# Performance work log

Measured on AMD Instinct MI355X. Metric: run time of the kernel, lower is better.

## Reference

```python
import jax, jax.numpy as jnp
import numpy as np

V, D, L, H, HKV, E = 32000, 1024, 4, 16, 4, 4
HD = D // H
B, T = 2, 1024
EPS = 1e-6
ROPE_BASE = 10000.0


def setup_inputs() -> dict:
    key = jax.random.key(0)
    ks = jax.random.split(key, 9)
    s = 0.02
    return {
        "input_ids": jax.random.randint(ks[0], (B, T), 0, V),
        "token_emb": jax.random.normal(ks[1], (V, D), jnp.float32) * s,
        "ln1_w": jnp.ones((L, D), jnp.float32),
        "q_w": jax.random.normal(ks[2], (L, D, D), jnp.float32) * s,
        "k_w": jax.random.normal(ks[3], (L, HKV * HD, D), jnp.float32) * s,
        "v_w": jax.random.normal(ks[4], (L, HKV * HD, D), jnp.float32) * s,
        "o_w": jax.random.normal(ks[5], (L, D, D), jnp.float32) * s,
        "ln2_w": jnp.ones((L, D), jnp.float32),
        "w1_w": jax.random.normal(ks[6], (L, E * D, D), jnp.float32) * s,
        "w2_w": jax.random.normal(ks[7], (L, D, E * D), jnp.float32) * s,
        "w3_w": jax.random.normal(ks[8], (L, E * D, D), jnp.float32) * s,
        "lnf_w": jnp.ones((D,), jnp.float32),
    }


def rmsnorm(x, w):
    var = jnp.mean(x * x, axis=-1, keepdims=True)
    return w * (x * jax.lax.rsqrt(var + EPS))


def rope_tables(t, dtype):
    inv_freq = 1.0 / (ROPE_BASE ** (jnp.arange(0, HD, 2, dtype=jnp.float32) / HD))
    freqs = jnp.outer(jnp.arange(t, dtype=jnp.float32), inv_freq)  # [T, HD/2]
    emb = jnp.concatenate([freqs, freqs], axis=-1)  # [T, HD]
    return emb.astype(dtype)[None, None], None  # placeholder shape helper


def rotate_half(x):
    x1, x2 = x[..., : HD // 2], x[..., HD // 2 :]
    return jnp.concatenate([-x2, x1], axis=-1)


def block(x, cos, sin, ln1, wq, wk, wv, wo, ln2, w1, w2, w3):
    # attention (pre-norm)
    h = rmsnorm(x, ln1)
    q = jnp.einsum('btd,ed->bte', h, wq).reshape(B, T, H, HD).transpose(0, 2, 1, 3)
    k = jnp.einsum('btd,ed->bte', h, wk).reshape(B, T, HKV, HD).transpose(0, 2, 1, 3)
    v = jnp.einsum('btd,ed->bte', h, wv).reshape(B, T, HKV, HD).transpose(0, 2, 1, 3)
    q = q * cos + rotate_half(q) * sin
    k = k * cos + rotate_half(k) * sin
    # GQA: repeat kv heads (repeat_interleave semantics)
    g = H // HKV
    k = jnp.repeat(k, g, axis=1)
    v = jnp.repeat(v, g, axis=1)
    scale = 1.0 / np.sqrt(HD)
    scores = jnp.einsum('bhqd,bhkd->bhqk', q, k) * scale
    causal = jnp.triu(jnp.ones((T, T), jnp.bool_), k=1)[None, None]
    scores = jnp.where(causal, -jnp.inf, scores)
    attn = jax.nn.softmax(scores.astype(jnp.float32), axis=-1).astype(q.dtype)
    o = jnp.einsum('bhqk,bhkd->bhqd', attn, v)
    o = o.transpose(0, 2, 1, 3).reshape(B, T, D)
    x = x + jnp.einsum('btd,ed->bte', o, wo)
    # SwiGLU FFN
    h = rmsnorm(x, ln2)
    gate = jax.nn.silu(jnp.einsum('btd,fd->btf', h, w1))
    up = jnp.einsum('btd,fd->btf', h, w3)
    x = x + jnp.einsum('btf,df->btd', gate * up, w2)
    return x


def forward(input_ids, token_emb, ln1_w, q_w, k_w, v_w, o_w, ln2_w, w1_w, w2_w, w3_w, lnf_w):
    x = token_emb[input_ids]  # [B,T,D]
    inv_freq = 1.0 / (ROPE_BASE ** (jnp.arange(0, HD, 2, dtype=jnp.float32) / HD))
    freqs = jnp.outer(jnp.arange(T, dtype=jnp.float32), inv_freq)
    emb = jnp.concatenate([freqs, freqs], axis=-1)  # [T, HD]
    cos = jnp.cos(emb)[None, None]  # [1,1,T,HD]
    sin = jnp.sin(emb)[None, None]
    for i in range(L):
        x = block(x, cos, sin, ln1_w[i], q_w[i], k_w[i], v_w[i], o_w[i],
                  ln2_w[i], w1_w[i], w2_w[i], w3_w[i])
    x = rmsnorm(x, lnf_w)
    logits = jnp.einsum('btd,vd->btv', x, token_emb)  # tied lm_head
    return logits


def reference(input_ids, token_emb, ln1_w, q_w, k_w, v_w, o_w, ln2_w, w1_w, w2_w, w3_w, lnf_w):
    return forward(input_ids, token_emb, ln1_w, q_w, k_w, v_w, o_w, ln2_w, w1_w, w2_w, w3_w, lnf_w)
```

## Files before the change

kernel.cpp:

```cpp
#include <hip/hip_runtime.h>
#include <math.h>

#define TT 1024
#define BB 2
#define DD 1024
#define NH 16
#define NKV 4
#define HD 64
#define ED 4096
#define LL 4
#define VV 32000
#define QKVS 1536

typedef __bf16 bf16x8 __attribute__((ext_vector_type(8)));
typedef float f32x4 __attribute__((ext_vector_type(4)));

__device__ inline unsigned short f2bf(float f) {
  unsigned u = __float_as_uint(f);
  u += 0x7fffu + ((u >> 16) & 1u);
  return (unsigned short)(u >> 16);
}

#define GLL16(gsrc, ldst)                                                            \
  __builtin_amdgcn_global_load_lds((const __attribute__((address_space(1))) void*)(gsrc), \
                                   (__attribute__((address_space(3))) void*)(ldst), 16, 0, 0)

__global__ void convw_kernel(const float* __restrict__ src, unsigned short* __restrict__ dst) {
  size_t i = (size_t)blockIdx.x * blockDim.x + threadIdx.x;
  float4 v = ((const float4*)src)[i];
  uint2 o;
  o.x = f2bf(v.x) | ((unsigned)f2bf(v.y) << 16);
  o.y = f2bf(v.z) | ((unsigned)f2bf(v.w) << 16);
  ((uint2*)dst)[i] = o;
}

__global__ void conv_qkv_kernel(const float* __restrict__ qw, const float* __restrict__ kw,
                                const float* __restrict__ vw, unsigned short* __restrict__ dst) {
  size_t i = (size_t)blockIdx.x * blockDim.x + threadIdx.x;
  size_t e = i * 4;
  int l = (int)(e / (QKVS * 1024));
  int rem = (int)(e - (size_t)l * (QKVS * 1024));
  int row = rem >> 10;
  int col = rem & 1023;
  const float* src;
  if (row < 1024) src = qw + (((size_t)l << 20) + ((size_t)row << 10)) + col;
  else if (row < 1280) src = kw + (((size_t)l << 18) + ((size_t)(row - 1024) << 10)) + col;
  else src = vw + (((size_t)l << 18) + ((size_t)(row - 1280) << 10)) + col;
  float4 v = *(const float4*)src;
  uint2 o;
  o.x = f2bf(v.x) | ((unsigned)f2bf(v.y) << 16);
  o.y = f2bf(v.z) | ((unsigned)f2bf(v.w) << 16);
  ((uint2*)dst)[i] = o;
}

__global__ void conv_w13_kernel(const float* __restrict__ w1, const float* __restrict__ w3,
                                unsigned short* __restrict__ dst) {
  size_t i = (size_t)blockIdx.x * blockDim.x + threadIdx.x;
  size_t e = i * 4;
  int l = (int)(e >> 23);
  int rem = (int)(e & ((1u << 23) - 1));
  int r = rem >> 10;
  int col = rem & 1023;
  int grp = r >> 4;
  int f = (grp >> 1) * 16 + (r & 15);
  const float* base = (grp & 1) ? w3 : w1;
  const float* src = base + (((size_t)l << 22) + ((size_t)f << 10)) + col;
  float4 v = *(const float4*)src;
  uint2 o;
  o.x = f2bf(v.x) | ((unsigned)f2bf(v.y) << 16);
  o.y = f2bf(v.z) | ((unsigned)f2bf(v.w) << 16);
  ((uint2*)dst)[i] = o;
}

__global__ void embed_kernel(const int* __restrict__ ids, const float* __restrict__ emb,
                             float* __restrict__ x) {
  int row = blockIdx.x;
  int id = ids[row];
  const float4* src = (const float4*)(emb + (size_t)id * DD);
  float4* dst = (float4*)(x + (size_t)row * DD);
  dst[threadIdx.x] = src[threadIdx.x];
}

__global__ __launch_bounds__(256) void rmsnorm_kernel(const float* __restrict__ x,
                                                      const float* __restrict__ wgt,
                                                      unsigned short* __restrict__ out) {
  int row = blockIdx.x;
  int tid = threadIdx.x;
  float4 v = *(const float4*)(x + (size_t)row * DD + tid * 4);
  float ss = v.x * v.x + v.y * v.y + v.z * v.z + v.w * v.w;
#pragma unroll
  for (int off = 32; off >= 1; off >>= 1) ss += __shfl_xor(ss, off);
  __shared__ float part[4];
  if ((tid & 63) == 0) part[tid >> 6] = ss;
  __syncthreads();
  ss = part[0] + part[1] + part[2] + part[3];
  float sc = rsqrtf(ss * (1.0f / DD) + 1e-6f);
  float4 wv = *(const float4*)(wgt + tid * 4);
  uint2 o;
  o.x = f2bf(v.x * wv.x * sc) | ((unsigned)f2bf(v.y * wv.y * sc) << 16);
  o.y = f2bf(v.z * wv.z * sc) | ((unsigned)f2bf(v.w * wv.w * sc) << 16);
  *(uint2*)(out + (size_t)row * DD + tid * 4) = o;
}

__global__ void add2_kernel(float* __restrict__ x, const float* __restrict__ p0,
                            const float* __restrict__ p1) {
  size_t i = (size_t)blockIdx.x * blockDim.x + threadIdx.x;
  float4 a = ((const float4*)x)[i];
  float4 b = ((const float4*)p0)[i];
  float4 c = ((const float4*)p1)[i];
  a.x += b.x + c.x; a.y += b.y + c.y; a.z += b.z + c.z; a.w += b.w + c.w;
  ((float4*)x)[i] = a;
}

template <int EPI>
__global__ __launch_bounds__(256) void gemm_bb(const unsigned short* __restrict__ A,
                                               const unsigned short* __restrict__ W,
                                               float* __restrict__ C,
                                               unsigned short* __restrict__ O2,
                                               int M, int N, int K) {
  __shared__ unsigned short As[128 * 32];
  __shared__ unsigned short Bs[128 * 32];
  const int tid = threadIdx.x;
  const int lane = tid & 63;
  const int w = tid >> 6;
  const int wm = (w >> 1) * 64;
  const int wn = (w & 1) * 64;
  const int l15 = lane & 15;
  const int quad = lane >> 4;
  const int q8 = quad * 8;

  const int nby = gridDim.y;
  const int nwg = gridDim.x * nby;
  const int bid = blockIdx.y * gridDim.x + blockIdx.x;
  int wk = bid;
  if ((nwg & 7) == 0) {
    int cpx = nwg >> 3;
    wk = (bid & 7) * cpx + (bid >> 3);
  }
  const int mBase = (wk % nby) * 128;
  const int nBase = (wk / nby) * 128;

  const int ksl = K / gridDim.z;
  const int kb0 = blockIdx.z * ksl;
  if (EPI == 0) C += (size_t)blockIdx.z * M * N;

  const unsigned short* Ab = A + (size_t)mBase * K;
  const unsigned short* Wb = W + (size_t)nBase * K;
  const int r0 = tid >> 2;
  const int c8 = (tid & 3) * 8;

  f32x4 acc[4][4] = {};

  for (int kt = kb0; kt < kb0 + ksl; kt += 32) {
    __syncthreads();
    GLL16(Ab + (size_t)r0 * K + kt + c8, As + (w * 64) * 8);
    GLL16(Ab + (size_t)(r0 + 64) * K + kt + c8, As + (256 + w * 64) * 8);
    GLL16(Wb + (size_t)r0 * K + kt + c8, Bs + (w * 64) * 8);
    GLL16(Wb + (size_t)(r0 + 64) * K + kt + c8, Bs + (256 + w * 64) * 8);
    __syncthreads();
    bf16x8 af[4], bfv[4];
#pragma unroll
    for (int ms = 0; ms < 4; ms++)
      af[ms] = *(const bf16x8*)&As[(wm + ms * 16 + l15) * 32 + q8];
#pragma unroll
    for (int ns = 0; ns < 4; ns++)
      bfv[ns] = *(const bf16x8*)&Bs[(wn + ns * 16 + l15) * 32 + q8];
#pragma unroll
    for (int ms = 0; ms < 4; ms++)
#pragma unroll
      for (int ns = 0; ns < 4; ns++)
        acc[ms][ns] = __builtin_amdgcn_mfma_f32_16x16x32_bf16(af[ms], bfv[ns], acc[ms][ns], 0, 0, 0);
  }

  if (EPI == 2) {
    const int fBase = ((nBase + wn) >> 5) * 16;
#pragma unroll
    for (int ms = 0; ms < 4; ms++)
#pragma unroll
      for (int r = 0; r < 4; r++) {
        int row = mBase + wm + ms * 16 + quad * 4 + r;
#pragma unroll
        for (int pp = 0; pp < 2; pp++) {
          float g = acc[ms][pp * 2][r];
          float u = acc[ms][pp * 2 + 1][r];
          float res = g / (1.f + __expf(-g)) * u;
          O2[(size_t)row * ED + fBase + pp * 16 + l15] = f2bf(res);
        }
      }
  } else if (EPI == 3) {
    const bool dorope = (nBase < 1280);
#pragma unroll
    for (int ms = 0; ms < 4; ms++)
#pragma unroll
      for (int r = 0; r < 4; r++) {
        int row = mBase + wm + ms * 16 + quad * 4 + r;
        float pos = (float)(row & (TT - 1));
#pragma unroll
        for (int ns = 0; ns < 2; ns++) {
          int col = nBase + wn + ns * 16 + l15;
          size_t i1 = (size_t)row * N + col;
          float x1 = acc[ms][ns][r], x2 = acc[ms][ns + 2][r];
          if (dorope) {
            int j = ns * 16 + l15;
            float invf = __expf(-(float)j * 0.28782313662f);
            float sv, cv;
            sincosf(pos * invf, &sv, &cv);
            C[i1] = x1 * cv - x2 * sv;
            C[i1 + 32] = x2 * cv + x1 * sv;
          } else {
            C[i1] = x1;
            C[i1 + 32] = x2;
          }
        }
      }
  } else {
#pragma unroll
    for (int ms = 0; ms < 4; ms++)
#pragma unroll
      for (int ns = 0; ns < 4; ns++)
#pragma unroll
        for (int r = 0; r < 4; r++) {
          int row = mBase + wm + ms * 16 + quad * 4 + r;
          int col = nBase + wn + ns * 16 + l15;
          size_t idx = (size_t)row * N + col;
          if (EPI == 0) C[idx] = acc[ms][ns][r];
          else if (EPI == 5) __builtin_nontemporal_store(acc[ms][ns][r], &C[idx]);
          else C[idx] += acc[ms][ns][r];
        }
  }
}

template <int EPI>
__global__ __launch_bounds__(256) void gemm_bt(const unsigned short* __restrict__ A,
                                               const float* __restrict__ W,
                                               float* __restrict__ C, int M, int N, int K) {
  __shared__ unsigned short As[128 * 40];
  __shared__ unsigned short Bs[128 * 40];
  const int tid = threadIdx.x;
  const int lane = tid & 63;
  const int w = tid >> 6;
  const int wm = (w >> 1) * 64;
  const int wn = (w & 1) * 64;
  const int l15 = lane & 15;
  const int quad = lane >> 4;
  const int q8 = quad * 8;

  const int nby = gridDim.y;
  const int nwg = gridDim.x * nby;
  const int bid = blockIdx.y * gridDim.x + blockIdx.x;
  int wk = bid;
  if ((nwg & 7) == 0) {
    int cpx = nwg >> 3;
    wk = (bid & 7) * cpx + (bid >> 3);
  }
  const int mBase = (wk % nby) * 128;
  const int nBase = (wk / nby) * 128;

  f32x4 acc[4][4] = {};

  for (int kt = 0; kt < K; kt += 32) {
    __syncthreads();
#pragma unroll
    for (int i = 0; i < 2; i++) {
      int chunk = tid + 256 * i;
      int r = chunk >> 2, cc8 = (chunk & 3) * 8;
      uint4 v = *(const uint4*)(A + (size_t)(mBase + r) * K + kt + cc8);
      *(uint4*)&As[r * 40 + cc8] = v;
    }
#pragma unroll
    for (int i = 0; i < 2; i++) {
      int chunk = tid + 256 * i;
      int r = chunk >> 2, cc8 = (chunk & 3) * 8;
      const float4* wp = (const float4*)(W + (size_t)(nBase + r) * K + kt + cc8);
      float4 f0 = wp[0], f1 = wp[1];
      uint4 v;
      v.x = f2bf(f0.x) | ((unsigned)f2bf(f0.y) << 16);
      v.y = f2bf(f0.z) | ((unsigned)f2bf(f0.w) << 16);
      v.z = f2bf(f1.x) | ((unsigned)f2bf(f1.y) << 16);
      v.w = f2bf(f1.z) | ((unsigned)f2bf(f1.w) << 16);
      *(uint4*)&Bs[r * 40 + cc8] = v;
    }
    __syncthreads();
    bf16x8 af[4], bfv[4];
#pragma unroll
    for (int ms = 0; ms < 4; ms++)
      af[ms] = *(const bf16x8*)&As[(wm + ms * 16 + l15) * 40 + q8];
#pragma unroll
    for (int ns = 0; ns < 4; ns++)
      bfv[ns] = *(const bf16x8*)&Bs[(wn + ns * 16 + l15) * 40 + q8];
#pragma unroll
    for (int ms = 0; ms < 4; ms++)
#pragma unroll
      for (int ns = 0; ns < 4; ns++)
        acc[ms][ns] = __builtin_amdgcn_mfma_f32_16x16x32_bf16(af[ms], bfv[ns], acc[ms][ns], 0, 0, 0);
  }
#pragma unroll
  for (int ms = 0; ms < 4; ms++)
#pragma unroll
    for (int ns = 0; ns < 4; ns++)
#pragma unroll
      for (int r = 0; r < 4; r++) {
        int row = mBase + wm + ms * 16 + quad * 4 + r;
        int col = nBase + wn + ns * 16 + l15;
        size_t idx = (size_t)row * N + col;
        if (EPI == 0) C[idx] = acc[ms][ns][r];
        else C[idx] += acc[ms][ns][r];
      }
}

__global__ __launch_bounds__(256) void attn_fwd(const float* __restrict__ Q,
                                                const float* __restrict__ Kb,
                                                const float* __restrict__ Vb,
                                                unsigned short* __restrict__ O) {
  __shared__ unsigned short Qs[64 * 72];
  __shared__ unsigned short Ks[64 * 72];
  __shared__ unsigned short Vt[64 * 72];
  const int tid = threadIdx.x;
  const int lane = tid & 63;
  const int w = tid >> 6;
  const int l15 = lane & 15;
  const int quad = lane >> 4;
  const int q8 = quad * 8;
  const int bh = blockIdx.x;
  const int b = bh / NH, h = bh % NH;
  const int hkv = h >> 2;
  const int qb = blockIdx.y;

#pragma unroll
  for (int i = 0; i < 4; i++) {
    int cc = tid + 256 * i;
    int r = cc >> 4, d4 = (cc & 15) * 4;
    float4 v = *(const float4*)(Q + (size_t)(b * TT + qb * 64 + r) * QKVS + h * HD + d4);
    uint2 p;
    p.x = f2bf(v.x) | ((unsigned)f2bf(v.y) << 16);
    p.y = f2bf(v.z) | ((unsigned)f2bf(v.w) << 16);
    *(uint2*)&Qs[r * 72 + d4] = p;
  }
  __syncthreads();
  bf16x8 qa0 = *(const bf16x8*)&Qs[(w * 16 + l15) * 72 + q8];
  bf16x8 qa1 = *(const bf16x8*)&Qs[(w * 16 + l15) * 72 + 32 + q8];

  f32x4 oacc[4] = {};
  float m_i[4], l_i[4];
#pragma unroll
  for (int r = 0; r < 4; r++) { m_i[r] = -1e30f; l_i[r] = 0.f; }

  for (int kb = 0; kb <= qb; kb++) {
    __syncthreads();
#pragma unroll
    for (int i = 0; i < 4; i++) {
      int cc = tid + 256 * i;
      int r = cc >> 4, d4 = (cc & 15) * 4;
      size_t grow = (size_t)(b * TT + kb * 64 + r) * QKVS + hkv * HD + d4;
      float4 kv = *(const float4*)(Kb + grow);
      uint2 p;
      p.x = f2bf(kv.x) | ((unsigned)f2bf(kv.y) << 16);
      p.y = f2bf(kv.z) | ((unsigned)f2bf(kv.w) << 16);
      *(uint2*)&Ks[r * 72 + d4] = p;
      float4 vv = *(const float4*)(Vb + grow);
      Vt[(d4 + 0) * 72 + r] = f2bf(vv.x);
      Vt[(d4 + 1) * 72 + r] = f2bf(vv.y);
      Vt[(d4 + 2) * 72 + r] = f2bf(vv.z);
      Vt[(d4 + 3) * 72 + r] = f2bf(vv.w);
    }
    __syncthreads();
    f32x4 s[4];
#pragma unroll
    for (int ns = 0; ns < 4; ns++) {
      bf16x8 k0 = *(const bf16x8*)&Ks[(ns * 16 + l15) * 72 + q8];
      bf16x8 k1 = *(const bf16x8*)&Ks[(ns * 16 + l15) * 72 + 32 + q8];
      f32x4 z = {};
      z = __builtin_amdgcn_mfma_f32_16x16x32_bf16(qa0, k0, z, 0, 0, 0);
      s[ns] = __builtin_amdgcn_mfma_f32_16x16x32_bf16(qa1, k1, z, 0, 0, 0);
    }
#pragma unroll
    for (int ns = 0; ns < 4; ns++)
#pragma unroll
      for (int r = 0; r < 4; r++) {
        float sv = s[ns][r] * 0.125f;
        if (kb == qb) {
          int qloc = w * 16 + quad * 4 + r;
          int kloc = ns * 16 + l15;
          if (kloc > qloc) sv = -1e30f;
        }
        s[ns][r] = sv;
      }
    float p[4][4];
    float alpha[4];
#pragma unroll
    for (int r = 0; r < 4; r++) {
      float mx = fmaxf(fmaxf(s[0][r], s[1][r]), fmaxf(s[2][r], s[3][r]));
#pragma unroll
      for (int off = 1; off < 16; off <<= 1) mx = fmaxf(mx, __shfl_xor(mx, off));
      float mnew = fmaxf(m_i[r], mx);
      alpha[r] = __expf(m_i[r] - mnew);
      float rs = 0.f;
#pragma unroll
      for (int ns = 0; ns < 4; ns++) {
        p[ns][r] = __expf(s[ns][r] - mnew);
        rs += p[ns][r];
      }
#pragma unroll
      for (int off = 1; off < 16; off <<= 1) rs += __shfl_xor(rs, off);
      l_i[r] = l_i[r] * alpha[r] + rs;
      m_i[r] = mnew;
    }
#pragma unroll
    for (int ds = 0; ds < 4; ds++)
#pragma unroll
      for (int r = 0; r < 4; r++) oacc[ds][r] *= alpha[r];
#pragma unroll
    for (int ns = 0; ns < 4; ns++)
#pragma unroll
      for (int r = 0; r < 4; r++)
        Qs[(w * 16 + quad * 4 + r) * 72 + ns * 16 + l15] = f2bf(p[ns][r]);
    __syncthreads();
    bf16x8 pa0 = *(const bf16x8*)&Qs[(w * 16 + l15) * 72 + q8];
    bf16x8 pa1 = *(const bf16x8*)&Qs[(w * 16 + l15) * 72 + 32 + q8];
#pragma unroll
    for (int ds = 0; ds < 4; ds++) {
      bf16x8 v0 = *(const bf16x8*)&Vt[(ds * 16 + l15) * 72 + q8];
      bf16x8 v1 = *(const bf16x8*)&Vt[(ds * 16 + l15) * 72 + 32 + q8];
      oacc[ds] = __builtin_amdgcn_mfma_f32_16x16x32_bf16(pa0, v0, oacc[ds], 0, 0, 0);
      oacc[ds] = __builtin_amdgcn_mfma_f32_16x16x32_bf16(pa1, v1, oacc[ds], 0, 0, 0);
    }
  }
#pragma unroll
  for (int ds = 0; ds < 4; ds++)
#pragma unroll
    for (int r = 0; r < 4; r++) {
      int row = qb * 64 + w * 16 + quad * 4 + r;
      int col = h * HD + ds * 16 + l15;
      O[(size_t)(b * TT + row) * DD + col] = f2bf(oacc[ds][r] / l_i[r]);
    }
}

extern "C" void kernel_launch(void* const* d_in, const int* in_sizes, int n_in,
                              void* d_out, int out_size, void* d_ws, size_t ws_size,
                              hipStream_t stream) {
  const int* ids = (const int*)d_in[0];
  const float* emb = (const float*)d_in[1];
  const float* ln1 = (const float*)d_in[2];
  const float* qw = (const float*)d_in[3];
  const float* kw = (const float*)d_in[4];
  const float* vw = (const float*)d_in[5];
  const float* ow = (const float*)d_in[6];
  const float* ln2 = (const float*)d_in[7];
  const float* w1 = (const float*)d_in[8];
  const float* w2 = (const float*)d_in[9];
  const float* w3 = (const float*)d_in[10];
  const float* lnf = (const float*)d_in[11];

  const int BT = BB * TT;
  const size_t MB = 1024ull * 1024ull;
  char* ob = (char*)d_out;

  float* guf = (float*)ob;
  unsigned short* hb2 = (unsigned short*)(ob + 64 * MB);
  unsigned short* qkvb = (unsigned short*)(ob + 80 * MB);
  unsigned short* owb = (unsigned short*)(ob + 92 * MB);
  unsigned short* w13b = (unsigned short*)(ob + 100 * MB);
  unsigned short* w2b = (unsigned short*)(ob + 164 * MB);

  char* wb = (char*)d_ws;
  unsigned short* hb = (unsigned short*)wb;
  float* x;
  float* qkv;
  unsigned short* ao;
  if (ws_size >= 28 * MB) {
    x = (float*)(wb + 4 * MB);
    qkv = (float*)(wb + 12 * MB);
    ao = (unsigned short*)(wb + 24 * MB);
  } else {
    x = (float*)(ob + 196 * MB);
    qkv = (float*)(ob + 204 * MB);
    ao = (unsigned short*)(ob + 216 * MB);
  }
  const bool bf16_logits = (ws_size >= 92 * MB);
  unsigned short* embb = bf16_logits ? (unsigned short*)(wb + 28 * MB) : nullptr;

  conv_qkv_kernel<<<6144, 256, 0, stream>>>(qw, kw, vw, qkvb);
  convw_kernel<<<4096, 256, 0, stream>>>(ow, owb);
  conv_w13_kernel<<<32768, 256, 0, stream>>>(w1, w3, w13b);
  convw_kernel<<<16384, 256, 0, stream>>>(w2, w2b);
  if (bf16_logits) convw_kernel<<<32000, 256, 0, stream>>>(emb, embb);

  embed_kernel<<<BT, 256, 0, stream>>>(ids, emb, x);
  float* p0 = guf;
  float* p1 = guf + (size_t)BT * DD;
  for (int l = 0; l < LL; l++) {
    rmsnorm_kernel<<<BT, 256, 0, stream>>>(x, ln1 + l * DD, hb);
    gemm_bb<3><<<dim3(QKVS / 128, BT / 128), 256, 0, stream>>>(
        hb, qkvb + (size_t)l * QKVS * DD, qkv, nullptr, BT, QKVS, DD);
    attn_fwd<<<dim3(BB * NH, TT / 64), 256, 0, stream>>>(qkv, qkv + 1024, qkv + 1280, ao);
    gemm_bb<1><<<dim3(DD / 128, BT / 128), 256, 0, stream>>>(
        ao, owb + (size_t)l * DD * DD, x, nullptr, BT, DD, DD);
    rmsnorm_kernel<<<BT, 256, 0, stream>>>(x, ln2 + l * DD, hb);
    gemm_bb<2><<<dim3((2 * ED) / 128, BT / 128), 256, 0, stream>>>(
        hb, w13b + (size_t)l * 2 * ED * DD, nullptr, hb2, BT, 2 * ED, DD);
    gemm_bb<0><<<dim3(DD / 128, BT / 128, 2), 256, 0, stream>>>(
        hb2, w2b + (size_t)l * DD * ED, p0, nullptr, BT, DD, ED);
    add2_kernel<<<(BT * DD / 4) / 256, 256, 0, stream>>>(x, p0, p1);
  }
  rmsnorm_kernel<<<BT, 256, 0, stream>>>(x, lnf, hb);
  if (bf16_logits) {
    gemm_bb<5><<<dim3(VV / 128, BT / 128), 256, 0, stream>>>(hb, embb, (float*)d_out, nullptr, BT, VV, DD);
  } else {
    gemm_bt<0><<<dim3(VV / 128, BT / 128), 256, 0, stream>>>(hb, emb, (float*)d_out, BT, VV, DD);
  }
}
```

Before: 1.843 ms.

## Add 256x256 eight-wave pipelined GEMM for FFN gate/up and logits

```diff
diff --git a/kernel.cpp b/kernel.cpp
--- a/kernel.cpp
+++ b/kernel.cpp
@@ -113,6 +113,156 @@
 }
 
 template <int EPI>
+__global__ __launch_bounds__(512) void gemm_8p(const unsigned short* __restrict__ A,
+                                               const unsigned short* __restrict__ W,
+                                               float* __restrict__ C,
+                                               unsigned short* __restrict__ O2,
+                                               int M, int N, int K) {
+  __shared__ unsigned short lds[49152];
+  const int tid = threadIdx.x;
+  const int lane = tid & 63;
+  const int w = tid >> 6;
+  const int wr = w >> 2;
+  const int wc = w & 3;
+  const int l15 = lane & 15;
+  const int quad = lane >> 4;
+  const int rq = ((quad ^ (l15 & 3)) << 3);
+  const int glr = lane >> 2;
+  const int gg8 = (((lane & 3) ^ ((lane >> 2) & 3)) << 3);
+
+  const int nby = gridDim.y;
+  const int nwg = gridDim.x * nby;
+  const int bid = blockIdx.y * gridDim.x + blockIdx.x;
+  int wk = bid;
+  if ((nwg & 7) == 0) { int cpx = nwg >> 3; wk = (bid & 7) * cpx + (bid >> 3); }
+  const int mBase = (wk % nby) * 256;
+  const int nBase = (wk / nby) * 256;
+
+  const unsigned short* gA0 = A + (size_t)(mBase + w * 16 + glr) * K + gg8;
+  const unsigned short* gA1 = A + (size_t)(mBase + 128 + w * 16 + glr) * K + gg8;
+  const unsigned short* gB0 = W + (size_t)(nBase + w * 16 + glr) * K + gg8;
+  const unsigned short* gB1 = W + (size_t)(nBase + 128 + w * 16 + glr) * K + gg8;
+
+#define STGA(SLOT, KOFF) do { \
+    GLL16(gA0 + (KOFF), &lds[(SLOT) * 8192 + w * 512]); \
+    GLL16(gA1 + (KOFF), &lds[(SLOT) * 8192 + 4096 + w * 512]); } while (0)
+#define STGB(SLOT, KOFF) do { \
+    GLL16(gB0 + (KOFF), &lds[24576 + (SLOT) * 8192 + w * 512]); \
+    GLL16(gB1 + (KOFF), &lds[24576 + (SLOT) * 8192 + 4096 + w * 512]); } while (0)
+#define LDA_(OFF, MH, MI) (*(const bf16x8*)&lds[(OFF) + (wr * 128 + (MH) * 64 + (MI) * 16 + l15) * 32 + rq])
+#define LDB_(OFF, NF)     (*(const bf16x8*)&lds[24576 + (OFF) + (wc * 64 + (NF) * 16 + l15) * 32 + rq])
+#define MM(MF, NF, AR, BR) acc[MF][NF] = __builtin_amdgcn_mfma_f32_16x16x32_bf16(AR, BR, acc[MF][NF], 0, 0, 0)
+#define MFMA16(MH) do { \
+    MM((MH)*4+0, 0, a0, b0); MM((MH)*4+0, 1, a0, b1); MM((MH)*4+0, 2, a0, b2); MM((MH)*4+0, 3, a0, b3); \
+    MM((MH)*4+1, 0, a1, b0); MM((MH)*4+1, 1, a1, b1); MM((MH)*4+1, 2, a1, b2); MM((MH)*4+1, 3, a1, b3); \
+    MM((MH)*4+2, 0, a2, b0); MM((MH)*4+2, 1, a2, b1); MM((MH)*4+2, 2, a2, b2); MM((MH)*4+2, 3, a2, b3); \
+    MM((MH)*4+3, 0, a3, b0); MM((MH)*4+3, 1, a3, b1); MM((MH)*4+3, 2, a3, b2); MM((MH)*4+3, 3, a3, b3); } while (0)
+#define CFENCE asm volatile("" ::: "memory")
+
+  f32x4 acc[8][4] = {};
+  int s0 = 0, s1 = 1;
+
+  STGA(0, 0); STGB(0, 0);
+  STGA(1, 32); STGB(1, 32);
+  CFENCE;
+  asm volatile("s_waitcnt vmcnt(4)" ::: "memory");
+  __builtin_amdgcn_s_barrier();
+
+  const int NT = K >> 6;
+  for (int t = 0; t < NT; ++t) {
+    const bool last = (t == NT - 1);
+    const int sn = 3 - s0 - s1;
+    const int ktn = (t + 1) << 6;
+    const int aoff0 = s0 * 8192, aoff1 = s1 * 8192;
+    bf16x8 a0, a1, a2, a3, b0, b1, b2, b3;
+
+    a0 = LDA_(aoff0, 0, 0); a1 = LDA_(aoff0, 0, 1); a2 = LDA_(aoff0, 0, 2); a3 = LDA_(aoff0, 0, 3);
+    b0 = LDB_(aoff0, 0); b1 = LDB_(aoff0, 1); b2 = LDB_(aoff0, 2); b3 = LDB_(aoff0, 3);
+    if (!last) { STGA(sn, ktn); STGB(sn, ktn); }
+    CFENCE;
+    __builtin_amdgcn_s_barrier();
+    __builtin_amdgcn_sched_barrier(0);
+    __builtin_amdgcn_s_setprio(1);
+    MFMA16(0);
+    __builtin_amdgcn_s_setprio(0);
+    CFENCE;
+    __builtin_amdgcn_s_barrier();
+
+    a0 = LDA_(aoff0, 1, 0); a1 = LDA_(aoff0, 1, 1); a2 = LDA_(aoff0, 1, 2); a3 = LDA_(aoff0, 1, 3);
+    CFENCE;
+    __builtin_amdgcn_s_barrier();
+    __builtin_amdgcn_sched_barrier(0);
+    __builtin_amdgcn_s_setprio(1);
+    MFMA16(1);
+    __builtin_amdgcn_s_setprio(0);
+    if (last) { asm volatile("s_waitcnt vmcnt(0)" ::: "memory"); }
+    else      { asm volatile("s_waitcnt vmcnt(4)" ::: "memory"); }
+    CFENCE;
+    __builtin_amdgcn_s_barrier();
+
+    a0 = LDA_(aoff1, 0, 0); a1 = LDA_(aoff1, 0, 1); a2 = LDA_(aoff1, 0, 2); a3 = LDA_(aoff1, 0, 3);
+    b0 = LDB_(aoff1, 0); b1 = LDB_(aoff1, 1); b2 = LDB_(aoff1, 2); b3 = LDB_(aoff1, 3);
+    if (!last) { STGA(s0, ktn + 32); STGB(s0, ktn + 32); }
+    CFENCE;
+    __builtin_amdgcn_s_barrier();
+    __builtin_amdgcn_sched_barrier(0);
+    __builtin_amdgcn_s_setprio(1);
+    MFMA16(0);
+    __builtin_amdgcn_s_setprio(0);
+    CFENCE;
+    __builtin_amdgcn_s_barrier();
+
+    a0 = LDA_(aoff1, 1, 0); a1 = LDA_(aoff1, 1, 1); a2 = LDA_(aoff1, 1, 2); a3 = LDA_(aoff1, 1, 3);
+    CFENCE;
+    __builtin_amdgcn_s_barrier();
+    __builtin_amdgcn_sched_barrier(0);
+    __builtin_amdgcn_s_setprio(1);
+    MFMA16(1);
+    __builtin_amdgcn_s_setprio(0);
+    if (!last) { asm volatile("s_waitcnt vmcnt(4)" ::: "memory"); }
+    CFENCE;
+    __builtin_amdgcn_s_barrier();
+
+    s1 = s0; s0 = sn;
+  }
+
+  if (EPI == 2) {
+    const int fBase = ((nBase + wc * 64) >> 5) * 16;
+#pragma unroll
+    for (int mf = 0; mf < 8; mf++)
+#pragma unroll
+      for (int rr = 0; rr < 4; rr++) {
+        int row = mBase + wr * 128 + mf * 16 + quad * 4 + rr;
+#pragma unroll
+        for (int pp = 0; pp < 2; pp++) {
+          float g = acc[mf][pp * 2][rr];
+          float u = acc[mf][pp * 2 + 1][rr];
+          float res = g / (1.f + __expf(-g)) * u;
+          O2[(size_t)row * ED + fBase + pp * 16 + l15] = f2bf(res);
+        }
+      }
+  } else {
+#pragma unroll
+    for (int mf = 0; mf < 8; mf++)
+#pragma unroll
+      for (int nf = 0; nf < 4; nf++)
+#pragma unroll
+        for (int rr = 0; rr < 4; rr++) {
+          int row = mBase + wr * 128 + mf * 16 + quad * 4 + rr;
+          int col = nBase + wc * 64 + nf * 16 + l15;
+          __builtin_nontemporal_store(acc[mf][nf][rr], &C[(size_t)row * N + col]);
+        }
+  }
+#undef STGA
+#undef STGB
+#undef LDA_
+#undef LDB_
+#undef MM
+#undef MFMA16
+#undef CFENCE
+}
+
+template <int EPI>
 __global__ __launch_bounds__(256) void gemm_bb(const unsigned short* __restrict__ A,
                                                const unsigned short* __restrict__ W,
                                                float* __restrict__ C,
@@ -172,22 +322,7 @@
         acc[ms][ns] = __builtin_amdgcn_mfma_f32_16x16x32_bf16(af[ms], bfv[ns], acc[ms][ns], 0, 0, 0);
   }
 
-  if (EPI == 2) {
-    const int fBase = ((nBase + wn) >> 5) * 16;
-#pragma unroll
-    for (int ms = 0; ms < 4; ms++)
-#pragma unroll
-      for (int r = 0; r < 4; r++) {
-        int row = mBase + wm + ms * 16 + quad * 4 + r;
-#pragma unroll
-        for (int pp = 0; pp < 2; pp++) {
-          float g = acc[ms][pp * 2][r];
-          float u = acc[ms][pp * 2 + 1][r];
-          float res = g / (1.f + __expf(-g)) * u;
-          O2[(size_t)row * ED + fBase + pp * 16 + l15] = f2bf(res);
-        }
-      }
-  } else if (EPI == 3) {
+  if (EPI == 3) {
     const bool dorope = (nBase < 1280);
 #pragma unroll
     for (int ms = 0; ms < 4; ms++)
@@ -224,7 +359,6 @@
           int col = nBase + wn + ns * 16 + l15;
           size_t idx = (size_t)row * N + col;
           if (EPI == 0) C[idx] = acc[ms][ns][r];
-          else if (EPI == 5) __builtin_nontemporal_store(acc[ms][ns][r], &C[idx]);
           else C[idx] += acc[ms][ns][r];
         }
   }
@@ -496,7 +630,7 @@
     gemm_bb<1><<<dim3(DD / 128, BT / 128), 256, 0, stream>>>(
         ao, owb + (size_t)l * DD * DD, x, nullptr, BT, DD, DD);
     rmsnorm_kernel<<<BT, 256, 0, stream>>>(x, ln2 + l * DD, hb);
-    gemm_bb<2><<<dim3((2 * ED) / 128, BT / 128), 256, 0, stream>>>(
+    gemm_8p<2><<<dim3((2 * ED) / 256, BT / 256), 512, 0, stream>>>(
         hb, w13b + (size_t)l * 2 * ED * DD, nullptr, hb2, BT, 2 * ED, DD);
     gemm_bb<0><<<dim3(DD / 128, BT / 128, 2), 256, 0, stream>>>(
         hb2, w2b + (size_t)l * DD * ED, p0, nullptr, BT, DD, ED);
@@ -504,7 +638,7 @@
   }
   rmsnorm_kernel<<<BT, 256, 0, stream>>>(x, lnf, hb);
   if (bf16_logits) {
-    gemm_bb<5><<<dim3(VV / 128, BT / 128), 256, 0, stream>>>(hb, embb, (float*)d_out, nullptr, BT, VV, DD);
+    gemm_8p<5><<<dim3(VV / 256, BT / 256), 512, 0, stream>>>(hb, embb, (float*)d_out, nullptr, BT, VV, DD);
   } else {
     gemm_bt<0><<<dim3(VV / 128, BT / 128), 256, 0, stream>>>(hb, emb, (float*)d_out, BT, VV, DD);
   }
```

After: 1.753 ms. 4.9% less time.
